# Performance work log

Measured on AMD Instinct MI355X. Metric: run time of the kernel, lower is better.

## Reference

```python
import jax, jax.numpy as jnp
import numpy as np

WINDOW = (16, 16)
STRIDE = (8, 8)
PADDING = (0, 0)  # (pad_h, pad_w), applied symmetrically like torch _pair semantics


def setup_inputs() -> dict:
    key = jax.random.key(0)
    x = jax.random.normal(key, (16, 3, 512, 512), dtype=jnp.float32)
    return {"x": x}


def reference(x) -> jnp.ndarray:
    wh, ww = WINDOW
    sh, sw = STRIDE
    ph, pw = PADDING
    if ph or pw:
        x = jnp.pad(x, ((0, 0), (0, 0), (ph, ph), (pw, pw)))
    B, C, H, W = x.shape
    nH = (H - wh) // sh + 1
    nW = (W - ww) // sw + 1
    # overlapping window gather indices
    rows = (jnp.arange(nH) * sh)[:, None] + jnp.arange(wh)[None, :]  # (nH, wh)
    cols = (jnp.arange(nW) * sw)[:, None] + jnp.arange(ww)[None, :]  # (nW, ww)
    # gather: (B, C, nH, nW, wh, ww)
    p = x[:, :, rows[:, None, :, None], cols[None, :, None, :]]
    # permute to (B, nH, nW, C, wh, ww) then flatten patch grid -> (B, N, C, wh, ww)
    p = jnp.transpose(p, (0, 2, 3, 1, 4, 5))
    return p.reshape(B, nH * nW, C, wh, ww)
```

## Files before the change

### kernel.cpp

```cpp
#include <hip/hip_runtime.h>


#define BB 16
#define CC 3
#define HH 512
#define WW 512
#define NH 63
#define NW 63
#define NP (NH * NW)

typedef float f4 __attribute__((ext_vector_type(4)));

__global__ __launch_bounds__(256) void scatter_patches_v8(
    const float* __restrict__ x, float* __restrict__ out) {
  unsigned int blk = blockIdx.x;
  unsigned int tid = threadIdx.x;

  unsigned int plane = blk >> 8;
  unsigned int b = plane / CC;
  unsigned int c = plane - b * CC;
  unsigned int row  = ((blk & 255u) << 1) | (tid >> 7);
  unsigned int col4 = tid & 127u;

  const f4* src = reinterpret_cast<const f4*>(x);
  f4 v = src[(plane << 16) + (row << 7) + col4];

  f4* o = reinterpret_cast<f4*>(out);
  unsigned int base = b * (NP * CC * 64u) + c * 64u;

  unsigned int ph1 = row >> 3;
  unsigned int i1  = row & 7u;
  unsigned int a1 = base + ph1 * (NW * CC * 64u) + (i1 << 2);
  unsigned int a2 = a1 - (NW * CC * 64u) + 32u;

  unsigned int offA = (col4 >> 1) * (CC * 64u) + (col4 & 1u);
  unsigned int offB = offA - (CC * 64u) + 2u;

  bool r1 = row < (HH - 8u);
  bool r2 = row >= 8u;
  bool ca = col4 < 126u;
  bool cb = col4 >= 2u;

  if (r1 & ca) o[a1 + offA] = v;
  if (r1 & cb) o[a1 + offB] = v;
  if (r2 & ca) o[a2 + offA] = v;
  if (r2 & cb) o[a2 + offB] = v;
}

extern "C" void kernel_launch(void* const* d_in, const int* in_sizes, int n_in,
                              void* d_out, int out_size, void* d_ws, size_t ws_size,
                              hipStream_t stream) {
  const float* x = (const float*)d_in[0];
  float* out = (float*)d_out;
  scatter_patches_v8<<<dim3(BB * CC * 256), 256, 0, stream>>>(x, out);
}
```

Measured before the change: 256.1 us.

## Replace input-driven scatter with output-driven gather and XCD-aware block remap

```diff
diff --git a/kernel.cpp b/kernel.cpp
--- a/kernel.cpp
+++ b/kernel.cpp
@@ -3,48 +3,36 @@
 
 #define BB 16
 #define CC 3
-#define HH 512
-#define WW 512
 #define NH 63
 #define NW 63
 #define NP (NH * NW)
+#define TOTAL_F4 (BB * NP * CC * 64u)
+#define NBLK 47632u
 
 typedef float f4 __attribute__((ext_vector_type(4)));
 
-__global__ __launch_bounds__(256) void scatter_patches_v8(
+__global__ __launch_bounds__(256) void gather_patches_v9(
     const float* __restrict__ x, float* __restrict__ out) {
-  unsigned int blk = blockIdx.x;
-  unsigned int tid = threadIdx.x;
+  unsigned blk = blockIdx.x;
+  unsigned id = (blk & 7u) * (NBLK / 8u) + (blk >> 3);
 
-  unsigned int plane = blk >> 8;
-  unsigned int b = plane / CC;
-  unsigned int c = plane - b * CC;
-  unsigned int row  = ((blk & 255u) << 1) | (tid >> 7);
-  unsigned int col4 = tid & 127u;
+  unsigned e = id * 256u + threadIdx.x;
+  if (e >= TOTAL_F4) return;
 
-  const f4* src = reinterpret_cast<const f4*>(x);
-  f4 v = src[(plane << 16) + (row << 7) + col4];
+  unsigned q = e >> 6;
+  unsigned r = e & 63u;
+  unsigned t = q / 3u;
+  unsigned c = q - t * 3u;
+  unsigned b = t / 3969u;
+  unsigned p = t - b * 3969u;
+  unsigned ph = p / 63u;
+  unsigned pw = p - ph * 63u;
 
-  f4* o = reinterpret_cast<f4*>(out);
-  unsigned int base = b * (NP * CC * 64u) + c * 64u;
+  unsigned srcidx = ((b * 3u + c) << 16)
+                  + ((8u * ph + (r >> 2)) << 7)
+                  + 2u * pw + (r & 3u);
 
-  unsigned int ph1 = row >> 3;
-  unsigned int i1  = row & 7u;
-  unsigned int a1 = base + ph1 * (NW * CC * 64u) + (i1 << 2);
-  unsigned int a2 = a1 - (NW * CC * 64u) + 32u;
-
-  unsigned int offA = (col4 >> 1) * (CC * 64u) + (col4 & 1u);
-  unsigned int offB = offA - (CC * 64u) + 2u;
-
-  bool r1 = row < (HH - 8u);
-  bool r2 = row >= 8u;
-  bool ca = col4 < 126u;
-  bool cb = col4 >= 2u;
-
-  if (r1 & ca) o[a1 + offA] = v;
-  if (r1 & cb) o[a1 + offB] = v;
-  if (r2 & ca) o[a2 + offA] = v;
-  if (r2 & cb) o[a2 + offB] = v;
+  reinterpret_cast<f4*>(out)[e] = reinterpret_cast<const f4*>(x)[srcidx];
 }
 
 extern "C" void kernel_launch(void* const* d_in, const int* in_sizes, int n_in,
@@ -52,5 +40,5 @@
                               hipStream_t stream) {
   const float* x = (const float*)d_in[0];
   float* out = (float*)d_out;
-  scatter_patches_v8<<<dim3(BB * CC * 256), 256, 0, stream>>>(x, out);
+  gather_patches_v9<<<dim3(NBLK), 256, 0, stream>>>(x, out);
 }
```

New measurement: 241.7 us. -5.6%, faster.
